# Optimization experiments

Hardware: AMD Instinct MI355X
Metric: run time of the kernel (lower is better)

Reference implementation:

```python
import jax, jax.numpy as jnp
import numpy as np
from jax import lax

EPS = 1e-6
BLOCK_SIZE = 64


def _feature_map(x, W):
    # x: (B,H,N,S,D), W: (H,D,F) -> (B,H,N,S,2F), computed in fp32
    u = jnp.einsum('bhnsd,hdf->bhnsf', x, W).astype(jnp.float32)
    return jnp.concatenate([jax.nn.softmax(u, axis=-1), jax.nn.softmax(-u, axis=-1)], axis=-1)


def setup_inputs() -> dict:
    key = jax.random.key(0)
    k1, k2, k3, k4, k5 = jax.random.split(key, 5)
    B, H, L, D, F = 2, 16, 4096, 64, 64
    q = jax.random.normal(k1, (B, H, L, D), dtype=jnp.float32)
    k = jax.random.normal(k2, (B, H, L, D), dtype=jnp.float32)
    v = jax.random.normal(k3, (B, H, L, D), dtype=jnp.float32)
    # hedgehog_weights initialized as eye(D,F) per head, perturbed so the test is non-trivial
    W = jnp.eye(D, F, dtype=jnp.float32)[None].repeat(H, axis=0) + 0.02 * jax.random.normal(k4, (H, D, F), dtype=jnp.float32)
    alpha = 0.1 * jax.random.normal(k5, (1, H, 1, 1), dtype=jnp.float32)
    return {"query_states": q, "key_states": k, "value_states": v,
            "hedgehog_weights": W, "alpha": alpha}


def _forward(q, k, v, W, alpha):
    B, H, L, D = q.shape
    S = BLOCK_SIZE
    N = L // S  # L chosen divisible by block size (no padding path)
    scaling = D ** (-0.5)
    F2 = 2 * W.shape[-1]

    qb = q.reshape(B, H, N, S, D)
    kb = k.reshape(B, H, N, S, D)
    vb = v.reshape(B, H, N, S, D)
    phi_q = _feature_map(qb, W)  # (B,H,N,S,2F) fp32
    phi_k = _feature_map(kb, W)
    w = jax.nn.sigmoid(alpha)    # (1,H,1,1)

    def step(carry, xs):
        S_state, Z_state = carry            # (B,H,2F,D), (B,H,2F)
        qn, kn, vn, pqn, pkn = xs           # per-block slices
        # linear-attention branch (pre-update state = clean history)
        lin_num = jnp.einsum('bhsf,bhfd->bhsd', pqn, S_state)
        lin_den = jnp.maximum(jnp.einsum('bhsf,bhf->bhs', pqn, Z_state)[..., None], EPS)
        # intra-block softmax branch (unnormalized, shared denominator)
        scores = jnp.einsum('bhsd,bhtd->bhst', qn, kn) * scaling
        a = jnp.exp(scores - scores.max(axis=-1, keepdims=True))
        sm_num = jnp.einsum('bhst,bhtd->bhsd', a, vn)
        sm_den = jnp.maximum(a.sum(axis=-1, keepdims=True), EPS)
        out = (w * sm_num + lin_num) / jnp.maximum(w * sm_den + lin_den, EPS)
        # state update with this block's keys/values
        S_state = S_state + jnp.einsum('bhsf,bhsd->bhfd', pkn, vn)
        Z_state = Z_state + pkn.sum(axis=-2)
        return (S_state, Z_state), out

    init = (jnp.zeros((B, H, F2, D), jnp.float32), jnp.zeros((B, H, F2), jnp.float32))
    xs = (jnp.moveaxis(qb, 2, 0), jnp.moveaxis(kb, 2, 0), jnp.moveaxis(vb, 2, 0),
          jnp.moveaxis(phi_q, 2, 0), jnp.moveaxis(phi_k, 2, 0))
    _, outs = lax.scan(step, init, xs)       # (N,B,H,S,D)
    return jnp.moveaxis(outs, 0, 2).reshape(B, H, L, D)


def reference(query_states, key_states, value_states, hedgehog_weights, alpha):
    return _forward(query_states, key_states, value_states, hedgehog_weights, alpha)
```

## Files before the change

### kernel.cpp

```cpp
#include <hip/hip_runtime.h>
#include <hip/hip_bf16.h>
#include <math.h>

constexpr int Hc = 16, Lc = 4096, Dc = 64;
constexpr int F2 = 128;
constexpr int NBLK = 2048;
constexpr float EPSf = 1e-6f;
constexpr float SCALE = 0.125f;

typedef short short8 __attribute__((ext_vector_type(8)));
typedef float f32x4 __attribute__((ext_vector_type(4)));
typedef unsigned short ushort;
typedef unsigned int uint;
typedef ushort ushort4v __attribute__((ext_vector_type(4)));

__device__ inline ushort f2bf(float x) {
    return __builtin_bit_cast(ushort, __float2bfloat16(x));
}
__device__ inline float bf2f(ushort h) {
    return __builtin_bit_cast(float, ((unsigned)h) << 16);
}
__device__ inline f32x4 zero4() { f32x4 z = {0.f, 0.f, 0.f, 0.f}; return z; }

__device__ inline f32x4 mfma(short8 a, short8 b, f32x4 c) {
    return __builtin_amdgcn_mfma_f32_16x16x32_bf16(a, b, c, 0, 0, 0);
}

__device__ inline void dma16(const void* g, void* l) {
    __builtin_amdgcn_global_load_lds(
        (const __attribute__((address_space(1))) unsigned int*)g,
        (__attribute__((address_space(3))) unsigned int*)l, 16, 0, 0);
}

__device__ inline short8 ldfrag(const char* L, int row, int chunk, int rowbytes, int mask) {
    return *(const short8*)(L + row * rowbytes + ((chunk * 16) ^ ((row & mask) << 4)));
}

__device__ inline short8 gfrag_f32(const float* __restrict__ base, int row, int chunk) {
    const float4* p = (const float4*)(base + row * 64 + chunk * 8);
    float4 a = p[0], b = p[1];
    short8 r;
    r[0] = (short)f2bf(a.x); r[1] = (short)f2bf(a.y); r[2] = (short)f2bf(a.z); r[3] = (short)f2bf(a.w);
    r[4] = (short)f2bf(b.x); r[5] = (short)f2bf(b.y); r[6] = (short)f2bf(b.z); r[7] = (short)f2bf(b.w);
    return r;
}
__device__ inline short8 gfrag_bf16(const ushort* __restrict__ base, int row, int chunk, int rowlen) {
    return *(const short8*)(base + row * rowlen + chunk * 8);
}

__device__ inline void stage_tr(const float* __restrict__ src, char* dst, int t) {
    int j = t & 63, g = t >> 6;
    #pragma unroll
    for (int i = 0; i < 4; ++i) {
        int i0 = g * 4 + i * 16;
        ushort4v hv;
        #pragma unroll
        for (int jj = 0; jj < 4; ++jj) hv[jj] = f2bf(src[(i0 + jj) * 64 + j]);
        *(ushort4v*)(dst + j * 128 + ((2 * i0) ^ ((j & 7) << 4))) = hv;
    }
}

__global__ __launch_bounds__(256) void passW(const float* __restrict__ W,
                                             ushort* __restrict__ Wt)
{
    const int h = blockIdx.x, t = threadIdx.x;
    const int f = t & 63, g = t >> 6;
    const float* src = W + (long)h * 4096;
    ushort* dst = Wt + (long)h * 4096;
    #pragma unroll
    for (int i = 0; i < 16; ++i) {
        int d = g * 16 + i;
        dst[f * 64 + d] = f2bf(src[d * 64 + f]);
    }
}

__global__ __launch_bounds__(256) void passA(const float* __restrict__ K,
                                             const float* __restrict__ V,
                                             const ushort* __restrict__ Wt,
                                             ushort* __restrict__ wsS,
                                             float* __restrict__ wsZ,
                                             char* __restrict__ wsV,
                                             char* __restrict__ wsK)
{
    __shared__ __align__(16) char lds[26624];
    char* vT = lds;
    char* pT = lds + 8192;
    float* Zp = (float*)(lds + 24576);

    const int t = threadIdx.x, wv = t >> 6, l = t & 63, lr = l & 15, lg = l >> 4;
    const int bid = blockIdx.x, bh = bid >> 6, h = bh & (Hc - 1);
    const long base = (long)bh * (Lc * Dc) + (long)(bid & 63) * (64 * Dc);

    stage_tr(V + base, vT, t);

    const float* kp = K + base;
    const ushort* wt = Wt + (long)h * 4096;

    short8 ak0 = gfrag_f32(kp, 16 * wv + lr, lg);
    short8 ak1 = gfrag_f32(kp, 16 * wv + lr, 4 + lg);

    {
        char* kd = wsK + (long)bid * 8192;
        const int srow = 16 * wv + lr;
        *(short8*)(kd + srow * 128 + ((lg * 16) ^ ((srow & 7) << 4))) = ak0;
        *(short8*)(kd + srow * 128 + (((4 + lg) * 16) ^ ((srow & 7) << 4))) = ak1;
    }

    f32x4 u0[4];
    #pragma unroll
    for (int tf = 0; tf < 4; ++tf) u0[tf] = zero4();
    #pragma unroll
    for (int tf = 0; tf < 4; ++tf) {
        u0[tf] = mfma(ak0, gfrag_bf16(wt, tf * 16 + lr, lg, 64), u0[tf]);
        u0[tf] = mfma(ak1, gfrag_bf16(wt, tf * 16 + lr, 4 + lg, 64), u0[tf]);
    }

    float pp[4][4], pn[4][4];
    float zpa[4] = {0.f,0.f,0.f,0.f}, zna[4] = {0.f,0.f,0.f,0.f};
    #pragma unroll
    for (int r = 0; r < 4; ++r) {
        float sp = 0.f, sn = 0.f;
        #pragma unroll
        for (int tf = 0; tf < 4; ++tf) {
            pp[tf][r] = __expf(u0[tf][r]);  sp += pp[tf][r];
            pn[tf][r] = __expf(-u0[tf][r]); sn += pn[tf][r];
        }
        #pragma unroll
        for (int m = 1; m < 16; m <<= 1) { sp += __shfl_xor(sp, m, 16); sn += __shfl_xor(sn, m, 16); }
        float rp = 1.f / sp, rn = 1.f / sn;
        #pragma unroll
        for (int tf = 0; tf < 4; ++tf) {
            pp[tf][r] *= rp; pn[tf][r] *= rn;
            zpa[tf] += pp[tf][r]; zna[tf] += pn[tf][r];
        }
    }

    const int s0 = 16 * wv + lg * 4;
    #pragma unroll
    for (int tf = 0; tf < 4; ++tf) {
        int f = tf * 16 + lr;
        ushort4v hp, hn;
        #pragma unroll
        for (int r = 0; r < 4; ++r) { hp[r] = f2bf(pp[tf][r]); hn[r] = f2bf(pn[tf][r]); }
        *(ushort4v*)(pT + f * 128 + ((2 * s0) ^ ((f & 7) << 4))) = hp;
        int fn = 64 + f;
        *(ushort4v*)(pT + fn * 128 + ((2 * s0) ^ ((fn & 7) << 4))) = hn;
    }
    #pragma unroll
    for (int tf = 0; tf < 4; ++tf) {
        zpa[tf] += __shfl_xor(zpa[tf], 16); zpa[tf] += __shfl_xor(zpa[tf], 32);
        zna[tf] += __shfl_xor(zna[tf], 16); zna[tf] += __shfl_xor(zna[tf], 32);
    }
    if (l < 16) {
        #pragma unroll
        for (int tf = 0; tf < 4; ++tf) {
            Zp[wv * 128 + tf * 16 + lr]      = zpa[tf];
            Zp[wv * 128 + 64 + tf * 16 + lr] = zna[tf];
        }
    }
    __syncthreads();

    {
        const short8* vs = (const short8*)vT;
        short8* vd = (short8*)(wsV + (long)bid * 8192);
        vd[t]       = vs[t];
        vd[t + 256] = vs[t + 256];
    }

    short8 av0 = ldfrag(vT, 16 * wv + lr, lg, 128, 7);
    short8 av1 = ldfrag(vT, 16 * wv + lr, 4 + lg, 128, 7);
    f32x4 acc[8];
    #pragma unroll
    for (int tf = 0; tf < 8; ++tf) acc[tf] = zero4();
    __builtin_amdgcn_s_setprio(1);
    #pragma unroll
    for (int tf = 0; tf < 8; ++tf) {
        acc[tf] = mfma(av0, ldfrag(pT, tf * 16 + lr, lg, 128, 7), acc[tf]);
        acc[tf] = mfma(av1, ldfrag(pT, tf * 16 + lr, 4 + lg, 128, 7), acc[tf]);
    }
    __builtin_amdgcn_s_setprio(0);
    ushort* o = wsS + (long)bid * (F2 * Dc);
    #pragma unroll
    for (int tf = 0; tf < 8; ++tf)
        #pragma unroll
        for (int r = 0; r < 4; ++r) {
            int d = 16 * wv + lg * 4 + r;
            o[d * 128 + tf * 16 + lr] = f2bf(acc[tf][r]);
        }

    if (t < 128)
        wsZ[(long)bid * F2 + t] = Zp[t] + Zp[128 + t] + Zp[256 + t] + Zp[384 + t];
}

__global__ __launch_bounds__(256) void passB(uint* __restrict__ wsSu,
                                             float* __restrict__ wsZ)
{
    const int t = threadIdx.x;
    if (blockIdx.x >= 512) {
        const int bh = blockIdx.x - 512;
        if (t < 128) {
            float zc = 0.f, zb[32];
            #pragma unroll
            for (int h2 = 0; h2 < 2; ++h2) {
                float* zp = wsZ + ((long)bh * 64 + h2 * 32) * 128 + t;
                #pragma unroll
                for (int i = 0; i < 32; ++i) zb[i] = zp[i * 128];
                #pragma unroll
                for (int i = 0; i < 32; ++i) { float x = zb[i]; zp[i * 128] = zc; zc += x; }
            }
        }
        return;
    }
    const int bh = blockIdx.x >> 4;
    const int slice = (blockIdx.x & 15) * 4 + (t >> 6);
    const int lane = t & 63;
    uint* p = wsSu + (long)bh * 64 * 4096 + slice * 64 + lane;
    uint buf[64];
    #pragma unroll
    for (int i = 0; i < 64; ++i) buf[i] = p[i * 4096];
    float c0 = 0.f, c1 = 0.f;
    #pragma unroll
    for (int i = 0; i < 64; ++i) {
        uint x = buf[i];
        uint pc = ((uint)f2bf(c1) << 16) | (uint)f2bf(c0);
        p[i * 4096] = pc;
        c0 += bf2f((ushort)(x & 0xffffu));
        c1 += bf2f((ushort)(x >> 16));
    }
}

__global__ __launch_bounds__(256, 5) void passC(const float* __restrict__ Q,
                                                const ushort* __restrict__ Wt,
                                                const float* __restrict__ Alpha,
                                                const ushort* __restrict__ wsS,
                                                const float* __restrict__ wsZ,
                                                const char* __restrict__ wsV,
                                                const char* __restrict__ wsK,
                                                float* __restrict__ Out)
{
    __shared__ __align__(16) char lds[32768];
    char* kR   = lds;
    char* aAB  = lds;
    char* phiH = lds;
    char* vT   = lds + 8192;
    char* St   = lds + 16384;

    const int t = threadIdx.x, wv = t >> 6, l = t & 63, lr = l & 15, lg = l >> 4;
    const int bid = blockIdx.x, bh = bid >> 6, h = bh & (Hc - 1);
    const long base = (long)bh * (Lc * Dc) + (long)(bid & 63) * (64 * Dc);
    const int s = 16 * wv + lr;

    {
        const char* kg = wsK + (long)bid * 8192;
        const char* vg = wsV + (long)bid * 8192;
        #pragma unroll
        for (int i = 0; i < 2; ++i) {
            int jb = wv * 128 + i * 64;
            dma16(kg + (long)(jb + l) * 16, kR + jb * 16);
            dma16(vg + (long)(jb + l) * 16, vT + jb * 16);
        }
        const char* sg = (const char*)(wsS + (long)bid * 8192);
        #pragma unroll
        for (int i = 0; i < 4; ++i) {
            int jb = wv * 256 + i * 64;
            int j = jb + l;
            int srcc = (j & ~15) | ((j & 15) ^ ((j >> 4) & 15));
            dma16(sg + (long)srcc * 16, St + jb * 16);
        }
    }

    const float* qp = Q + base;
    short8 bq0 = gfrag_f32(qp, s, lg);
    short8 bq1 = gfrag_f32(qp, s, 4 + lg);
    const ushort* wt = Wt + (long)h * 4096;
    short8 aw[4][2];
    #pragma unroll
    for (int tf = 0; tf < 4; ++tf) {
        aw[tf][0] = gfrag_bf16(wt, tf * 16 + lr, lg, 64);
        aw[tf][1] = gfrag_bf16(wt, tf * 16 + lr, 4 + lg, 64);
    }
    float4 zv4[4], zn4[4];
    {
        const float* zp = wsZ + (long)bid * 128;
        #pragma unroll
        for (int tf = 0; tf < 4; ++tf) {
            zv4[tf] = *(const float4*)(zp + tf * 16 + lg * 4);
            zn4[tf] = *(const float4*)(zp + 64 + tf * 16 + lg * 4);
        }
    }

    f32x4 uq[4];
    #pragma unroll
    for (int tf = 0; tf < 4; ++tf) uq[tf] = zero4();
    #pragma unroll
    for (int tf = 0; tf < 4; ++tf) {
        uq[tf] = mfma(aw[tf][0], bq0, uq[tf]);
        uq[tf] = mfma(aw[tf][1], bq1, uq[tf]);
    }

    float sp = 0.f, sn = 0.f;
    float pqp[4][4], pqn[4][4];
    #pragma unroll
    for (int tf = 0; tf < 4; ++tf)
        #pragma unroll
        for (int r = 0; r < 4; ++r) {
            pqp[tf][r] = __expf(uq[tf][r]);  sp += pqp[tf][r];
            pqn[tf][r] = __expf(-uq[tf][r]); sn += pqn[tf][r];
        }
    sp += __shfl_xor(sp, 16); sp += __shfl_xor(sp, 32);
    sn += __shfl_xor(sn, 16); sn += __shfl_xor(sn, 32);
    ushort4v phk[4], phkn[4];
    {
        float rp = 1.f / sp, rn = 1.f / sn;
        #pragma unroll
        for (int tf = 0; tf < 4; ++tf)
            #pragma unroll
            for (int r = 0; r < 4; ++r) {
                phk[tf][r]  = f2bf(pqp[tf][r] * rp);
                phkn[tf][r] = f2bf(pqn[tf][r] * rn);
            }
    }
    const float w = 1.f / (1.f + __expf(-Alpha[h]));

    float zd = 0.f;
    #pragma unroll
    for (int tf = 0; tf < 4; ++tf)
        #pragma unroll
        for (int r = 0; r < 4; ++r)
            zd += bf2f(phk[tf][r]) * (&zv4[tf].x)[r] + bf2f(phkn[tf][r]) * (&zn4[tf].x)[r];
    zd += __shfl_xor(zd, 16); zd += __shfl_xor(zd, 32);
    const float lden = fmaxf(zd, EPSf);

    __syncthreads();

    f32x4 sc[4];
    #pragma unroll
    for (int tt = 0; tt < 4; ++tt) sc[tt] = zero4();
    __builtin_amdgcn_s_setprio(1);
    #pragma unroll
    for (int tt = 0; tt < 4; ++tt) {
        sc[tt] = mfma(ldfrag(kR, tt * 16 + lr, lg, 128, 7), bq0, sc[tt]);
        sc[tt] = mfma(ldfrag(kR, tt * 16 + lr, 4 + lg, 128, 7), bq1, sc[tt]);
    }
    __builtin_amdgcn_s_setprio(0);
    #pragma unroll
    for (int tt = 0; tt < 4; ++tt)
        #pragma unroll
        for (int r = 0; r < 4; ++r) sc[tt][r] *= SCALE;
    float m2;
    {
        float m01 = fmaxf(fmaxf(fmaxf(sc[0][0], sc[0][1]), fmaxf(sc[0][2], sc[0][3])),
                          fmaxf(fmaxf(sc[1][0], sc[1][1]), fmaxf(sc[1][2], sc[1][3])));
        float m23 = fmaxf(fmaxf(fmaxf(sc[2][0], sc[2][1]), fmaxf(sc[2][2], sc[2][3])),
                          fmaxf(fmaxf(sc[3][0], sc[3][1]), fmaxf(sc[3][2], sc[3][3])));
        m2 = fmaxf(m01, m23);
        m2 = fmaxf(m2, __shfl_xor(m2, 16));
        m2 = fmaxf(m2, __shfl_xor(m2, 32));
    }
    float as = 0.f;
    ushort4v apk[4];
    #pragma unroll
    for (int tt = 0; tt < 4; ++tt)
        #pragma unroll
        for (int r = 0; r < 4; ++r) {
            float e = __expf(sc[tt][r] - m2);
            as += e;
            apk[tt][r] = f2bf(w * e);
        }
    as += __shfl_xor(as, 16); as += __shfl_xor(as, 32);
    const float sden = fmaxf(as, EPSf);
    const float inv = 1.f / fmaxf(w * sden + lden, EPSf);

    __syncthreads();

    #pragma unroll
    for (int tt = 0; tt < 4; ++tt)
        *(ushort4v*)(aAB + s * 128 + ((32 * tt + 8 * lg) ^ ((s & 7) << 4))) = apk[tt];
    short8 aa0 = ldfrag(aAB, s, lg, 128, 7);
    short8 aa1 = ldfrag(aAB, s, 4 + lg, 128, 7);

    f32x4 oacc[4];
    #pragma unroll
    for (int td = 0; td < 4; ++td) oacc[td] = zero4();
    __builtin_amdgcn_s_setprio(1);
    #pragma unroll
    for (int td = 0; td < 4; ++td) {
        oacc[td] = mfma(aa0, ldfrag(vT, td * 16 + lr, lg, 128, 7), oacc[td]);
        oacc[td] = mfma(aa1, ldfrag(vT, td * 16 + lr, 4 + lg, 128, 7), oacc[td]);
    }
    __builtin_amdgcn_s_setprio(0);

    #pragma unroll
    for (int tf = 0; tf < 4; ++tf)
        *(ushort4v*)(phiH + s * 128 + ((32 * tf + 8 * lg) ^ ((s & 7) << 4))) = phk[tf];
    {
        short8 pf0 = ldfrag(phiH, s, lg, 128, 7);
        short8 pf1 = ldfrag(phiH, s, 4 + lg, 128, 7);
        __builtin_amdgcn_s_setprio(1);
        #pragma unroll
        for (int td = 0; td < 4; ++td) {
            oacc[td] = mfma(pf0, ldfrag(St, td * 16 + lr, lg, 256, 15), oacc[td]);
            oacc[td] = mfma(pf1, ldfrag(St, td * 16 + lr, 4 + lg, 256, 15), oacc[td]);
        }
        __builtin_amdgcn_s_setprio(0);
    }
    #pragma unroll
    for (int tf = 0; tf < 4; ++tf)
        *(ushort4v*)(phiH + s * 128 + ((32 * tf + 8 * lg) ^ ((s & 7) << 4))) = phkn[tf];
    {
        short8 pn0 = ldfrag(phiH, s, lg, 128, 7);
        short8 pn1 = ldfrag(phiH, s, 4 + lg, 128, 7);
        __builtin_amdgcn_s_setprio(1);
        #pragma unroll
        for (int td = 0; td < 4; ++td) {
            oacc[td] = mfma(pn0, ldfrag(St, td * 16 + lr, 8 + lg, 256, 15), oacc[td]);
            oacc[td] = mfma(pn1, ldfrag(St, td * 16 + lr, 12 + lg, 256, 15), oacc[td]);
        }
        __builtin_amdgcn_s_setprio(0);
    }

    float* op = Out + base;
    #pragma unroll
    for (int r = 0; r < 4; ++r) {
        float invr = __shfl(inv, lg * 4 + r, 16);
        int sr = 16 * wv + lg * 4 + r;
        #pragma unroll
        for (int td = 0; td < 4; ++td)
            op[sr * 64 + td * 16 + lr] = oacc[td][r] * invr;
    }
}

extern "C" void kernel_launch(void* const* d_in, const int* in_sizes, int n_in,
                              void* d_out, int out_size, void* d_ws, size_t ws_size,
                              hipStream_t stream)
{
    const float* q     = (const float*)d_in[0];
    const float* k     = (const float*)d_in[1];
    const float* v     = (const float*)d_in[2];
    const float* W     = (const float*)d_in[3];
    const float* alpha = (const float*)d_in[4];
    float* out = (float*)d_out;

    ushort* wsSb = (ushort*)d_ws;
    float*  wsZ  = (float*)((char*)d_ws + (size_t)NBLK * F2 * Dc * 2);
    ushort* Wtb  = (ushort*)((char*)wsZ + (size_t)NBLK * F2 * 4);
    char*   wsV  = (char*)Wtb + (size_t)Hc * 4096 * 2;
    char*   wsK  = wsV + (size_t)NBLK * 8192;

    passW<<<Hc, 256, 0, stream>>>(W, Wtb);
    passA<<<NBLK, 256, 0, stream>>>(k, v, Wtb, wsSb, wsZ, wsV, wsK);
    passB<<<544, 256, 0, stream>>>((uint*)wsSb, wsZ);
    passC<<<NBLK, 256, 0, stream>>>(q, Wtb, alpha, wsSb, wsZ, wsV, wsK, out);
}
```

Measured before the change: 70.92 us.

## Interleave K/V workspace, reorder passC loads, use partial vmcnt waits at barriers

Stores K and V bf16 tiles for each block contiguously in a single interleaved workspace. passC now issues the Q, W and Z register loads before the async LDS DMAs, and replaces the two __syncthreads with explicit s_waitcnt vmcnt counts plus raw barriers. The first barrier waits only for the K and V DMAs, so the state-tile DMA can keep running during the score computation. This relies on the vmcnt(6) count matching the outstanding-load order the compiler actually emits; a mismatch would be a race.

```diff
diff --git a/kernel.cpp b/kernel.cpp
--- a/kernel.cpp
+++ b/kernel.cpp
@@ -79,8 +79,7 @@
                                              const ushort* __restrict__ Wt,
                                              ushort* __restrict__ wsS,
                                              float* __restrict__ wsZ,
-                                             char* __restrict__ wsV,
-                                             char* __restrict__ wsK)
+                                             char* __restrict__ wsKV)
 {
     __shared__ __align__(16) char lds[26624];
     char* vT = lds;
@@ -100,7 +99,7 @@
     short8 ak1 = gfrag_f32(kp, 16 * wv + lr, 4 + lg);
 
     {
-        char* kd = wsK + (long)bid * 8192;
+        char* kd = wsKV + (long)bid * 16384;
         const int srow = 16 * wv + lr;
         *(short8*)(kd + srow * 128 + ((lg * 16) ^ ((srow & 7) << 4))) = ak0;
         *(short8*)(kd + srow * 128 + (((4 + lg) * 16) ^ ((srow & 7) << 4))) = ak1;
@@ -162,7 +161,7 @@
 
     {
         const short8* vs = (const short8*)vT;
-        short8* vd = (short8*)(wsV + (long)bid * 8192);
+        short8* vd = (short8*)(wsKV + (long)bid * 16384 + 8192);
         vd[t]       = vs[t];
         vd[t + 256] = vs[t + 256];
     }
@@ -234,8 +233,7 @@
                                                 const float* __restrict__ Alpha,
                                                 const ushort* __restrict__ wsS,
                                                 const float* __restrict__ wsZ,
-                                                const char* __restrict__ wsV,
-                                                const char* __restrict__ wsK,
+                                                const char* __restrict__ wsKV,
                                                 float* __restrict__ Out)
 {
     __shared__ __align__(16) char lds[32768];
@@ -250,13 +248,37 @@
     const long base = (long)bh * (Lc * Dc) + (long)(bid & 63) * (64 * Dc);
     const int s = 16 * wv + lr;
 
-    {
-        const char* kg = wsK + (long)bid * 8192;
-        const char* vg = wsV + (long)bid * 8192;
+    const float* qp = Q + base;
+    short8 bq0 = gfrag_f32(qp, s, lg);
+    short8 bq1 = gfrag_f32(qp, s, 4 + lg);
+    const ushort* wt = Wt + (long)h * 4096;
+    short8 aw[4][2];
+    #pragma unroll
+    for (int tf = 0; tf < 4; ++tf) {
+        aw[tf][0] = gfrag_bf16(wt, tf * 16 + lr, lg, 64);
+        aw[tf][1] = gfrag_bf16(wt, tf * 16 + lr, 4 + lg, 64);
+    }
+    float4 zv4[4], zn4[4];
+    {
+        const float* zp = wsZ + (long)bid * 128;
+        #pragma unroll
+        for (int tf = 0; tf < 4; ++tf) {
+            zv4[tf] = *(const float4*)(zp + tf * 16 + lg * 4);
+            zn4[tf] = *(const float4*)(zp + 64 + tf * 16 + lg * 4);
+        }
+    }
+
+    {
+        const char* kg = wsKV + (long)bid * 16384;
         #pragma unroll
         for (int i = 0; i < 2; ++i) {
             int jb = wv * 128 + i * 64;
             dma16(kg + (long)(jb + l) * 16, kR + jb * 16);
+        }
+        const char* vg = kg + 8192;
+        #pragma unroll
+        for (int i = 0; i < 2; ++i) {
+            int jb = wv * 128 + i * 64;
             dma16(vg + (long)(jb + l) * 16, vT + jb * 16);
         }
         const char* sg = (const char*)(wsS + (long)bid * 8192);
@@ -266,26 +288,6 @@
             int j = jb + l;
             int srcc = (j & ~15) | ((j & 15) ^ ((j >> 4) & 15));
             dma16(sg + (long)srcc * 16, St + jb * 16);
-        }
-    }
-
-    const float* qp = Q + base;
-    short8 bq0 = gfrag_f32(qp, s, lg);
-    short8 bq1 = gfrag_f32(qp, s, 4 + lg);
-    const ushort* wt = Wt + (long)h * 4096;
-    short8 aw[4][2];
-    #pragma unroll
-    for (int tf = 0; tf < 4; ++tf) {
-        aw[tf][0] = gfrag_bf16(wt, tf * 16 + lr, lg, 64);
-        aw[tf][1] = gfrag_bf16(wt, tf * 16 + lr, 4 + lg, 64);
-    }
-    float4 zv4[4], zn4[4];
-    {
-        const float* zp = wsZ + (long)bid * 128;
-        #pragma unroll
-        for (int tf = 0; tf < 4; ++tf) {
-            zv4[tf] = *(const float4*)(zp + tf * 16 + lg * 4);
-            zn4[tf] = *(const float4*)(zp + 64 + tf * 16 + lg * 4);
         }
     }
 
@@ -331,7 +333,9 @@
     zd += __shfl_xor(zd, 16); zd += __shfl_xor(zd, 32);
     const float lden = fmaxf(zd, EPSf);
 
-    __syncthreads();
+    asm volatile("s_waitcnt vmcnt(6)" ::: "memory");
+    __builtin_amdgcn_s_barrier();
+    __builtin_amdgcn_sched_barrier(0);
 
     f32x4 sc[4];
     #pragma unroll
@@ -371,7 +375,9 @@
     const float sden = fmaxf(as, EPSf);
     const float inv = 1.f / fmaxf(w * sden + lden, EPSf);
 
-    __syncthreads();
+    asm volatile("s_waitcnt vmcnt(0)" ::: "memory");
+    __builtin_amdgcn_s_barrier();
+    __builtin_amdgcn_sched_barrier(0);
 
     #pragma unroll
     for (int tt = 0; tt < 4; ++tt)
@@ -444,11 +450,10 @@
     ushort* wsSb = (ushort*)d_ws;
     float*  wsZ  = (float*)((char*)d_ws + (size_t)NBLK * F2 * Dc * 2);
     ushort* Wtb  = (ushort*)((char*)wsZ + (size_t)NBLK * F2 * 4);
-    char*   wsV  = (char*)Wtb + (size_t)Hc * 4096 * 2;
-    char*   wsK  = wsV + (size_t)NBLK * 8192;
+    char*   wsKV = (char*)Wtb + (size_t)Hc * 4096 * 2;
 
     passW<<<Hc, 256, 0, stream>>>(W, Wtb);
-    passA<<<NBLK, 256, 0, stream>>>(k, v, Wtb, wsSb, wsZ, wsV, wsK);
+    passA<<<NBLK, 256, 0, stream>>>(k, v, Wtb, wsSb, wsZ, wsKV);
     passB<<<544, 256, 0, stream>>>((uint*)wsSb, wsZ);
-    passC<<<NBLK, 256, 0, stream>>>(q, Wtb, alpha, wsSb, wsZ, wsV, wsK, out);
-}
+    passC<<<NBLK, 256, 0, stream>>>(q, Wtb, alpha, wsSb, wsZ, wsKV, out);
+}
```

Measured after the change: 71.30 us. No clear change (+0.5%).
